# Kernel optimization log

Measured on AMD Instinct MI355X. Metric: run time of the kernel, lower is better.

## Reference

```python
import jax, jax.numpy as jnp
from jax import lax
import numpy as np

EPS = 1e-5
ALPHA = 0.2  # LeakyReLU slope


def setup_inputs() -> dict:
    key = jax.random.key(0)
    ks = jax.random.split(key, 8)
    B, N, F_IN, HID, OUT, H = 32, 512, 256, 512, 512, 4
    D = OUT // H
    return {
        "x": jax.random.normal(ks[0], (B, N, F_IN), dtype=jnp.float32),
        "adj": jax.random.uniform(ks[1], (N, N), dtype=jnp.float32),
        "gc_w": jax.random.normal(ks[2], (F_IN, HID), dtype=jnp.float32) * 0.04,
        "gc_b": jax.random.normal(ks[3], (HID,), dtype=jnp.float32) * 0.04,
        "bn1_g": jnp.ones((HID,), jnp.float32),
        "bn1_b": jnp.zeros((HID,), jnp.float32),
        "bn1_m": jnp.zeros((HID,), jnp.float32),
        "bn1_v": jnp.ones((HID,), jnp.float32),
        "gat_w": jax.random.normal(ks[4], (H, D, HID), dtype=jnp.float32) * 0.04,
        "conv_w": jax.random.normal(ks[5], (OUT, OUT, 3), dtype=jnp.float32) * 0.02,
        "conv_b": jax.random.normal(ks[6], (OUT,), dtype=jnp.float32) * 0.02,
        "bn2_g": jnp.ones((OUT,), jnp.float32),
        "bn2_b": jnp.zeros((OUT,), jnp.float32),
        "bn2_m": jnp.zeros((OUT,), jnp.float32),
        "bn2_v": jnp.ones((OUT,), jnp.float32),
    }


def reference(x, adj, gc_w, gc_b, bn1_g, bn1_b, bn1_m, bn1_v, gat_w,
              conv_w, conv_b, bn2_g, bn2_b, bn2_m, bn2_v):
    # --- GraphConvolution: adj @ (x @ W) + b ---
    support = jnp.einsum('bnc,cd->bnd', x, gc_w)
    g = jnp.einsum('nm,bmd->bnd', adj, support) + gc_b  # [B,N,HID]
    # --- BatchNorm1d over channel dim (eval mode) + ReLU ---
    g = (g - bn1_m) * (bn1_g / jnp.sqrt(bn1_v + EPS)) + bn1_b
    g = jax.nn.relu(g)
    # --- Multi-head GAT (repeat/mul/sum == attention-weighted matmul) ---
    hh = jnp.einsum('bnf,hdf->bhnd', g, gat_w)           # per-head projections
    e = jnp.einsum('bhnd,bhmd->bhnm', hh, hh)            # logits [B,H,N,N]
    e = jnp.where(e > 0, e, ALPHA * e)                   # LeakyReLU
    att = jax.nn.softmax(e, axis=-1)
    o = jnp.einsum('bhnm,bhmd->bhnd', att, hh)
    B, H, N, D = o.shape
    o = o.transpose(0, 2, 1, 3).reshape(B, N, H * D)     # concat heads [B,N,OUT]
    # --- TCN block: conv1d(k=3,pad=1) over node axis + BN(eval) + ReLU ---
    xc = o.transpose(0, 2, 1)                            # [B,C,N]
    y = lax.conv_general_dilated(xc, conv_w, (1,), ((1, 1),),
                                 dimension_numbers=('NCH', 'OIH', 'NCH'))
    y = y + conv_b[None, :, None]
    y = (y - bn2_m[None, :, None]) * (bn2_g / jnp.sqrt(bn2_v + EPS))[None, :, None] + bn2_b[None, :, None]
    y = jax.nn.relu(y)
    return y.transpose(0, 2, 1)                          # [B,N,OUT]
```

## Files before the change

kernel.cpp:

```cpp
#include <hip/hip_runtime.h>
#include <math.h>

#define BATCH 32
#define NNODE 512
#define FIN   256
#define HIDC  512
#define OUTC  512
#define NHEAD 4
#define HDIM  128
#define EPSV  1e-5f
#define ALPHA_LR 0.2f

typedef _Float16 half8 __attribute__((ext_vector_type(8)));
typedef _Float16 half4v __attribute__((ext_vector_type(4)));
typedef float floatx4 __attribute__((ext_vector_type(4)));

#define GLOBAL_TO_LDS16(g, l)                                                  \
  __builtin_amdgcn_global_load_lds(                                            \
      (const __attribute__((address_space(1))) void*)(g),                      \
      (__attribute__((address_space(3))) void*)(l), 16, 0, 0)

__device__ __forceinline__ void split_gemm_acc(
    const _Float16* __restrict__ Ah, const _Float16* __restrict__ Al, int lda,
    const _Float16* __restrict__ Bh, const _Float16* __restrict__ Bl, int ldb,
    int K, int rowBase, int colBase,
    _Float16* sAh, _Float16* sAl, _Float16* sBh, _Float16* sBl,
    floatx4 acc[4][4], int tid) {
  const int lane = tid & 63, wave = tid >> 6;
  const int wr = (wave >> 1) * 64, wc = (wave & 1) * 64;
  const int fr = lane & 15, q = lane >> 4;
  const int r = tid >> 2, ko = (tid & 3) * 8;
  for (int k0 = 0; k0 < K; k0 += 32) {
    GLOBAL_TO_LDS16(&Ah[(size_t)(rowBase + r) * lda + k0 + ko], &sAh[tid * 8]);
    GLOBAL_TO_LDS16(&Ah[(size_t)(rowBase + r + 64) * lda + k0 + ko], &sAh[2048 + tid * 8]);
    GLOBAL_TO_LDS16(&Al[(size_t)(rowBase + r) * lda + k0 + ko], &sAl[tid * 8]);
    GLOBAL_TO_LDS16(&Al[(size_t)(rowBase + r + 64) * lda + k0 + ko], &sAl[2048 + tid * 8]);
    GLOBAL_TO_LDS16(&Bh[(size_t)(colBase + r) * ldb + k0 + ko], &sBh[tid * 8]);
    GLOBAL_TO_LDS16(&Bh[(size_t)(colBase + r + 64) * ldb + k0 + ko], &sBh[2048 + tid * 8]);
    GLOBAL_TO_LDS16(&Bl[(size_t)(colBase + r) * ldb + k0 + ko], &sBl[tid * 8]);
    GLOBAL_TO_LDS16(&Bl[(size_t)(colBase + r + 64) * ldb + k0 + ko], &sBl[2048 + tid * 8]);
    __syncthreads();
    half8 ah[4], al4[4], bh[4], bl4[4];
#pragma unroll
    for (int i = 0; i < 4; ++i) {
      ah[i]  = *(const half8*)&sAh[(wr + i * 16 + fr) * 32 + q * 8];
      al4[i] = *(const half8*)&sAl[(wr + i * 16 + fr) * 32 + q * 8];
    }
#pragma unroll
    for (int j = 0; j < 4; ++j) {
      bh[j]  = *(const half8*)&sBh[(wc + j * 16 + fr) * 32 + q * 8];
      bl4[j] = *(const half8*)&sBl[(wc + j * 16 + fr) * 32 + q * 8];
    }
#pragma unroll
    for (int i = 0; i < 4; ++i)
#pragma unroll
      for (int j = 0; j < 4; ++j) {
        acc[i][j] = __builtin_amdgcn_mfma_f32_16x16x32_f16(al4[i], bh[j], acc[i][j], 0, 0, 0);
        acc[i][j] = __builtin_amdgcn_mfma_f32_16x16x32_f16(ah[i], bl4[j], acc[i][j], 0, 0, 0);
        acc[i][j] = __builtin_amdgcn_mfma_f32_16x16x32_f16(ah[i], bh[j], acc[i][j], 0, 0, 0);
      }
    __syncthreads();
  }
}

__global__ __launch_bounds__(256) void k_prep(
    const float* __restrict__ adj, const float* __restrict__ gcw,
    const float* __restrict__ gatw, const float* __restrict__ cw,
    _Float16* __restrict__ ADJh, _Float16* __restrict__ ADJl,
    _Float16* __restrict__ GWh, _Float16* __restrict__ GWl,
    _Float16* __restrict__ GAh, _Float16* __restrict__ GAl,
    _Float16* __restrict__ WT, _Float16* __restrict__ OP) {
  const int i = blockIdx.x * 256 + threadIdx.x;
  if (i < 262144) {
    float v = adj[i];
    _Float16 h = (_Float16)v;
    ADJh[i] = h; ADJl[i] = (_Float16)(v - (float)h);
  } else if (i < 393216) {
    int j = i - 262144;
    int n = j >> 8, k = j & 255;
    float v = gcw[(size_t)k * HIDC + n];
    _Float16 h = (_Float16)v;
    GWh[j] = h; GWl[j] = (_Float16)(v - (float)h);
  } else if (i < 655360) {
    int j = i - 393216;
    float v = gatw[j];
    _Float16 h = (_Float16)v;
    GAh[j] = h; GAl[j] = (_Float16)(v - (float)h);
  } else if (i < 1441792) {
    int j = i - 655360;
    int n = j / 1536, kk = j - n * 1536;
    int tap = kk >> 9, ci = kk & 511;
    WT[j] = (_Float16)cw[(size_t)n * 1536 + ci * 3 + tap];
  } else if (i < 1474560) {
    int j = i - 1441792;
    int b = j >> 10, rs = (j >> 9) & 1, c = j & 511;
    OP[((size_t)b * 514 + rs * 513) * OUTC + c] = (_Float16)0.f;
  }
}

__global__ __launch_bounds__(256) void k_xsplit(const float* __restrict__ X,
                                                _Float16* __restrict__ Xh,
                                                _Float16* __restrict__ Xl) {
  const int i = (blockIdx.x * 256 + threadIdx.x) * 4;
  float4 v = *(const float4*)&X[i];
  half4v h, l;
  h[0] = (_Float16)v.x; l[0] = (_Float16)(v.x - (float)h[0]);
  h[1] = (_Float16)v.y; l[1] = (_Float16)(v.y - (float)h[1]);
  h[2] = (_Float16)v.z; l[2] = (_Float16)(v.z - (float)h[2]);
  h[3] = (_Float16)v.w; l[3] = (_Float16)(v.w - (float)h[3]);
  *(half4v*)&Xh[i] = h;
  *(half4v*)&Xl[i] = l;
}

__global__ __launch_bounds__(256) void k_support_t(
    const _Float16* __restrict__ GWh, const _Float16* __restrict__ GWl,
    const _Float16* __restrict__ Xh, const _Float16* __restrict__ Xl,
    _Float16* __restrict__ STh, _Float16* __restrict__ STl) {
  __shared__ _Float16 sm[4][4096];
  const int tid = threadIdx.x;
  const int rowBase = blockIdx.y * 128, colBase = blockIdx.x * 128;
  floatx4 acc[4][4] = {};
  split_gemm_acc(GWh, GWl, FIN, Xh, Xl, FIN, FIN, rowBase, colBase,
                 sm[0], sm[1], sm[2], sm[3], acc, tid);
  const int lane = tid & 63, wave = tid >> 6;
  const int wr = (wave >> 1) * 64, wc = (wave & 1) * 64;
  const int fr = lane & 15, q = lane >> 4;
#pragma unroll
  for (int i = 0; i < 4; ++i) {
    const int ch0 = rowBase + wr + i * 16 + q * 4;
#pragma unroll
    for (int rg = 0; rg < 4; ++rg) {
      size_t base = (size_t)(ch0 + rg) * 16384 + colBase + wc + fr;
#pragma unroll
      for (int j = 0; j < 4; ++j) {
        float v = acc[i][j][rg];
        _Float16 h = (_Float16)v;
        STh[base + j * 16] = h;
        STl[base + j * 16] = (_Float16)(v - (float)h);
      }
    }
  }
}

__global__ __launch_bounds__(256) void k_gcn(
    const _Float16* __restrict__ ADJh, const _Float16* __restrict__ ADJl,
    const _Float16* __restrict__ STh, const _Float16* __restrict__ STl,
    const float* __restrict__ gcb, const float* __restrict__ g1,
    const float* __restrict__ b1, const float* __restrict__ m1,
    const float* __restrict__ v1,
    _Float16* __restrict__ Gh, _Float16* __restrict__ Gl) {
  __shared__ _Float16 sm[4][4096];
  const int tid = threadIdx.x;
  const int rowBase = blockIdx.y * 128, colBase = blockIdx.x * 128;
  const int b = blockIdx.z;
  floatx4 acc[4][4] = {};
  split_gemm_acc(ADJh, ADJl, NNODE, STh + (size_t)b * NNODE, STl + (size_t)b * NNODE,
                 16384, NNODE, rowBase, colBase, sm[0], sm[1], sm[2], sm[3], acc, tid);
  const int lane = tid & 63, wave = tid >> 6;
  const int wr = (wave >> 1) * 64, wc = (wave & 1) * 64;
  const int fr = lane & 15, q = lane >> 4;
  float sc[4], of[4];
#pragma unroll
  for (int j = 0; j < 4; ++j) {
    int c = colBase + wc + j * 16 + fr;
    float s = g1[c] * rsqrtf(v1[c] + EPSV);
    sc[j] = s;
    of[j] = (gcb[c] - m1[c]) * s + b1[c];
  }
#pragma unroll
  for (int i = 0; i < 4; ++i) {
    const int n0 = rowBase + wr + i * 16 + q * 4;
#pragma unroll
    for (int rg = 0; rg < 4; ++rg) {
      size_t base = ((size_t)b * NNODE + n0 + rg) * HIDC + colBase + wc + fr;
#pragma unroll
      for (int j = 0; j < 4; ++j) {
        float v = fmaxf(fmaf(acc[i][j][rg], sc[j], of[j]), 0.0f);
        _Float16 h = (_Float16)v;
        Gh[base + j * 16] = h;
        Gl[base + j * 16] = (_Float16)(v - (float)h);
      }
    }
  }
}

__global__ __launch_bounds__(256) void k_hh(
    const _Float16* __restrict__ Gh, const _Float16* __restrict__ Gl,
    const _Float16* __restrict__ GAh, const _Float16* __restrict__ GAl,
    _Float16* __restrict__ HHh, _Float16* __restrict__ HHl) {
  __shared__ _Float16 sm[4][4096];
  const int tid = threadIdx.x;
  const int rowBase = blockIdx.y * 128, colBase = blockIdx.x * 128;
  floatx4 acc[4][4] = {};
  split_gemm_acc(Gh, Gl, HIDC, GAh, GAl, HIDC, HIDC, rowBase, colBase,
                 sm[0], sm[1], sm[2], sm[3], acc, tid);
  const int lane = tid & 63, wave = tid >> 6;
  const int wr = (wave >> 1) * 64, wc = (wave & 1) * 64;
  const int fr = lane & 15, q = lane >> 4;
#pragma unroll
  for (int i = 0; i < 4; ++i) {
    const int r0 = rowBase + wr + i * 16 + q * 4;
#pragma unroll
    for (int rg = 0; rg < 4; ++rg) {
      size_t base = (size_t)(r0 + rg) * OUTC + colBase + wc + fr;
#pragma unroll
      for (int j = 0; j < 4; ++j) {
        float v = acc[i][j][rg];
        _Float16 h = (_Float16)v;
        HHh[base + j * 16] = h;
        HHl[base + j * 16] = (_Float16)(v - (float)h);
      }
    }
  }
}

__global__ __launch_bounds__(256) void k_vt(const _Float16* __restrict__ HHh,
                                            _Float16* __restrict__ HHT) {
  __shared__ _Float16 sT[128 * 132];
  const int bt = blockIdx.x;
  const int nt = bt & 3, g = bt >> 2;
  const int bb = g >> 2, h = g & 3;
  const int tid = threadIdx.x;
  const int rr = tid >> 4, cc = (tid & 15) * 8;
#pragma unroll
  for (int it = 0; it < 8; ++it) {
    int node = rr + it * 16;
    half8 v = *(const half8*)&HHh[((size_t)bb * 512 + nt * 128 + node) * 512 + h * 128 + cc];
#pragma unroll
    for (int e = 0; e < 8; ++e) sT[(cc + e) * 132 + node] = v[e];
  }
  __syncthreads();
#pragma unroll
  for (int it = 0; it < 8; ++it) {
    int d = rr + it * 16;
    half8 v;
#pragma unroll
    for (int e = 0; e < 8; ++e) v[e] = sT[d * 132 + cc + e];
    *(half8*)&HHT[((size_t)g * 128 + d) * 512 + nt * 128 + cc] = v;
  }
}

__global__ __launch_bounds__(256, 3) void k_attn(
    const _Float16* __restrict__ HHh, const _Float16* __restrict__ HHl,
    const _Float16* __restrict__ HHT, _Float16* __restrict__ OP) {
  __shared__ _Float16 sKh[128 * 32], sKl[128 * 32];
  __shared__ _Float16 sV[128 * 32];
  __shared__ _Float16 sP[64 * 44];
  const int tid = threadIdx.x;
  const int lane = tid & 63, wave = tid >> 6;
  const int fr = lane & 15, q = lane >> 4;
  const int id = blockIdx.x;
  const int slot = id >> 3;
  const int g = (id & 7) + 8 * (slot >> 3);
  const int qBase = (slot & 7) * 64;
  const int bb = g >> 2, h = g & 3;
  const int w16 = wave * 16;
  const _Float16* Qh = HHh + (size_t)bb * NNODE * OUTC + h * HDIM;
  const _Float16* Ql = HHl + (size_t)bb * NNODE * OUTC + h * HDIM;
  const _Float16* VT = HHT + (size_t)g * HDIM * NNODE;
  const int r = tid >> 2, ko = (tid & 3) * 8;

  half8 qh[4], ql[4];
#pragma unroll
  for (int k0 = 0; k0 < 4; ++k0) {
    const size_t off = (size_t)(qBase + w16 + fr) * OUTC + k0 * 32 + q * 8;
    qh[k0] = *(const half8*)&Qh[off];
    ql[k0] = *(const half8*)&Ql[off];
  }

  floatx4 oacc[8] = {};
  float m_i[4], l_i[4];
#pragma unroll
  for (int rg = 0; rg < 4; ++rg) { m_i[rg] = -1e30f; l_i[rg] = 0.f; }

  for (int kt = 0; kt < 4; ++kt) {
    const int ktb = kt * 128;
    floatx4 sacc[8] = {};
#pragma unroll
    for (int k0 = 0; k0 < 4; ++k0) {
      GLOBAL_TO_LDS16(&Qh[(size_t)(ktb + r) * OUTC + k0 * 32 + ko], &sKh[tid * 8]);
      GLOBAL_TO_LDS16(&Qh[(size_t)(ktb + r + 64) * OUTC + k0 * 32 + ko], &sKh[2048 + tid * 8]);
      GLOBAL_TO_LDS16(&Ql[(size_t)(ktb + r) * OUTC + k0 * 32 + ko], &sKl[tid * 8]);
      GLOBAL_TO_LDS16(&Ql[(size_t)(ktb + r + 64) * OUTC + k0 * 32 + ko], &sKl[2048 + tid * 8]);
      __syncthreads();
#pragma unroll
      for (int j = 0; j < 8; ++j) {
        half8 bh = *(const half8*)&sKh[(j * 16 + fr) * 32 + q * 8];
        half8 bl = *(const half8*)&sKl[(j * 16 + fr) * 32 + q * 8];
        sacc[j] = __builtin_amdgcn_mfma_f32_16x16x32_f16(ql[k0], bh, sacc[j], 0, 0, 0);
        sacc[j] = __builtin_amdgcn_mfma_f32_16x16x32_f16(qh[k0], bl, sacc[j], 0, 0, 0);
        sacc[j] = __builtin_amdgcn_mfma_f32_16x16x32_f16(qh[k0], bh, sacc[j], 0, 0, 0);
      }
      __syncthreads();
    }
#pragma unroll
    for (int j = 0; j < 8; ++j)
#pragma unroll
      for (int rg = 0; rg < 4; ++rg) {
        float v = sacc[j][rg];
        sacc[j][rg] = v > 0.f ? v : ALPHA_LR * v;
      }
#pragma unroll
    for (int rg = 0; rg < 4; ++rg) {
      float mx = sacc[0][rg];
#pragma unroll
      for (int j = 1; j < 8; ++j) mx = fmaxf(mx, sacc[j][rg]);
      mx = fmaxf(mx, __shfl_xor(mx, 1));
      mx = fmaxf(mx, __shfl_xor(mx, 2));
      mx = fmaxf(mx, __shfl_xor(mx, 4));
      mx = fmaxf(mx, __shfl_xor(mx, 8));
      float mnew = fmaxf(m_i[rg], mx);
      float alpha = __expf(m_i[rg] - mnew);
      m_i[rg] = mnew;
      float sum = 0.f;
#pragma unroll
      for (int j = 0; j < 8; ++j) {
        float p = __expf(sacc[j][rg] - mnew);
        sacc[j][rg] = p;
        sum += p;
      }
      sum += __shfl_xor(sum, 1);
      sum += __shfl_xor(sum, 2);
      sum += __shfl_xor(sum, 4);
      sum += __shfl_xor(sum, 8);
      l_i[rg] = l_i[rg] * alpha + sum;
#pragma unroll
      for (int j = 0; j < 8; ++j) oacc[j][rg] *= alpha;
    }
#pragma unroll
    for (int ks = 0; ks < 4; ++ks) {
#pragma unroll
      for (int jj = 0; jj < 2; ++jj)
#pragma unroll
        for (int rg = 0; rg < 4; ++rg)
          sP[(w16 + q * 4 + rg) * 44 + jj * 16 + fr] = (_Float16)sacc[2 * ks + jj][rg];
      GLOBAL_TO_LDS16(&VT[(size_t)r * NNODE + ktb + ks * 32 + ko], &sV[tid * 8]);
      GLOBAL_TO_LDS16(&VT[(size_t)(r + 64) * NNODE + ktb + ks * 32 + ko], &sV[2048 + tid * 8]);
      __syncthreads();
      half8 pa = *(const half8*)&sP[(w16 + fr) * 44 + q * 8];
#pragma unroll
      for (int j = 0; j < 8; ++j) {
        half8 bv = *(const half8*)&sV[(j * 16 + fr) * 32 + q * 8];
        oacc[j] = __builtin_amdgcn_mfma_f32_16x16x32_f16(pa, bv, oacc[j], 0, 0, 0);
      }
      __syncthreads();
    }
  }
#pragma unroll
  for (int rg = 0; rg < 4; ++rg) {
    const float inv = 1.0f / l_i[rg];
    const int node = qBase + w16 + q * 4 + rg;
    size_t base = ((size_t)bb * 514 + 1 + node) * OUTC + h * HDIM + fr;
#pragma unroll
    for (int j = 0; j < 8; ++j)
      OP[base + j * 16] = (_Float16)(oacc[j][rg] * inv);
  }
}

__global__ __launch_bounds__(256) void k_conv_mfma(
    const _Float16* __restrict__ OP, const _Float16* __restrict__ WT,
    const float* __restrict__ cb, const float* __restrict__ g2,
    const float* __restrict__ b2, const float* __restrict__ m2,
    const float* __restrict__ v2, float* __restrict__ Y) {
  __shared__ _Float16 At[128 * 32];
  __shared__ _Float16 Bt[128 * 32];
  const int tid = threadIdx.x;
  const int lane = tid & 63, wave = tid >> 6;
  const int wr = (wave >> 1) * 64, wc = (wave & 1) * 64;
  const int id = blockIdx.y * 4 + blockIdx.x;
  const int jj = id >> 3;
  const int rowBase = ((id & 7) * 16 + (jj >> 2)) * 128;
  const int colBase = (jj & 3) * 128;
  const int b = rowBase >> 9;
  const int n0 = rowBase & 511;
  const int r = tid >> 2;
  const int ko = (tid & 3) * 8;
  floatx4 acc[4][4] = {};
  for (int k0 = 0; k0 < 3 * OUTC; k0 += 32) {
    const int tap = k0 >> 9;
    const int cib = k0 & 511;
    const size_t abase = ((size_t)b * 514 + n0 + tap) * OUTC + cib + ko;
    GLOBAL_TO_LDS16(&OP[abase + (size_t)r * OUTC],        &At[tid * 8]);
    GLOBAL_TO_LDS16(&OP[abase + (size_t)(r + 64) * OUTC], &At[2048 + tid * 8]);
    GLOBAL_TO_LDS16(&WT[(size_t)(colBase + r) * 1536 + k0 + ko],      &Bt[tid * 8]);
    GLOBAL_TO_LDS16(&WT[(size_t)(colBase + r + 64) * 1536 + k0 + ko], &Bt[2048 + tid * 8]);
    __syncthreads();
    const int fr = lane & 15, q = lane >> 4;
    half8 af[4], bf[4];
#pragma unroll
    for (int i = 0; i < 4; ++i)
      af[i] = *(const half8*)&At[(wr + i * 16 + fr) * 32 + q * 8];
#pragma unroll
    for (int j = 0; j < 4; ++j)
      bf[j] = *(const half8*)&Bt[(wc + j * 16 + fr) * 32 + q * 8];
#pragma unroll
    for (int i = 0; i < 4; ++i)
#pragma unroll
      for (int j = 0; j < 4; ++j)
        acc[i][j] = __builtin_amdgcn_mfma_f32_16x16x32_f16(af[i], bf[j], acc[i][j], 0, 0, 0);
    __syncthreads();
  }
  const int fr = lane & 15, q = lane >> 4;
  float sc[4], of[4];
#pragma unroll
  for (int j = 0; j < 4; ++j) {
    int c = colBase + wc + j * 16 + fr;
    float s = g2[c] * rsqrtf(v2[c] + EPSV);
    sc[j] = s;
    of[j] = (cb[c] - m2[c]) * s + b2[c];
  }
#pragma unroll
  for (int i = 0; i < 4; ++i) {
    const int R0r = rowBase + wr + i * 16 + q * 4;
#pragma unroll
    for (int rg = 0; rg < 4; ++rg) {
      float* dst = &Y[(size_t)(R0r + rg) * OUTC + colBase + wc + fr];
#pragma unroll
      for (int j = 0; j < 4; ++j)
        dst[j * 16] = fmaxf(fmaf(acc[i][j][rg], sc[j], of[j]), 0.0f);
    }
  }
}

extern "C" void kernel_launch(void* const* d_in, const int* in_sizes, int n_in,
                              void* d_out, int out_size, void* d_ws, size_t ws_size,
                              hipStream_t stream) {
  const float* x     = (const float*)d_in[0];
  const float* adj   = (const float*)d_in[1];
  const float* gc_w  = (const float*)d_in[2];
  const float* gc_b  = (const float*)d_in[3];
  const float* bn1_g = (const float*)d_in[4];
  const float* bn1_b = (const float*)d_in[5];
  const float* bn1_m = (const float*)d_in[6];
  const float* bn1_v = (const float*)d_in[7];
  const float* gat_w = (const float*)d_in[8];
  const float* conv_w= (const float*)d_in[9];
  const float* conv_b= (const float*)d_in[10];
  const float* bn2_g = (const float*)d_in[11];
  const float* bn2_b = (const float*)d_in[12];
  const float* bn2_m = (const float*)d_in[13];
  const float* bn2_v = (const float*)d_in[14];
  float* out = (float*)d_out;

  char* ws = (char*)d_ws;
  _Float16* STh = (_Float16*)(ws + 0);
  _Float16* STl = (_Float16*)(ws + 16777216);
  _Float16* HHh = (_Float16*)(ws + 0);
  _Float16* HHl = (_Float16*)(ws + 16777216);
  _Float16* Xh  = (_Float16*)(ws + 33554432);
  _Float16* Xl  = (_Float16*)(ws + 41943040);
  _Float16* Gh  = (_Float16*)(ws + 33554432);
  _Float16* Gl  = (_Float16*)(ws + 50331648);
  _Float16* HHT = (_Float16*)(ws + 33554432);
  _Float16* OP  = (_Float16*)(ws + 67108864);
  _Float16* WT  = (_Float16*)(ws + 83951616);
  _Float16* ADJh= (_Float16*)(ws + 85524480);
  _Float16* ADJl= (_Float16*)(ws + 86048768);
  _Float16* GWh = (_Float16*)(ws + 86573056);
  _Float16* GWl = (_Float16*)(ws + 86835200);
  _Float16* GAh = (_Float16*)(ws + 87097344);
  _Float16* GAl = (_Float16*)(ws + 87621632);

  k_prep<<<5760, 256, 0, stream>>>(adj, gc_w, gat_w, conv_w,
                                   ADJh, ADJl, GWh, GWl, GAh, GAl, WT, OP);
  k_xsplit<<<4096, 256, 0, stream>>>(x, Xh, Xl);
  k_support_t<<<dim3(128, 4), 256, 0, stream>>>(GWh, GWl, Xh, Xl, STh, STl);
  k_gcn<<<dim3(4, 4, 32), 256, 0, stream>>>(ADJh, ADJl, STh, STl, gc_b,
                                            bn1_g, bn1_b, bn1_m, bn1_v, Gh, Gl);
  k_hh<<<dim3(4, 128), 256, 0, stream>>>(Gh, Gl, GAh, GAl, HHh, HHl);
  k_vt<<<512, 256, 0, stream>>>(HHh, HHT);
  k_attn<<<1024, 256, 0, stream>>>(HHh, HHl, HHT, OP);
  k_conv_mfma<<<dim3(4, 128), 256, 0, stream>>>(OP, WT, conv_b,
                                                bn2_g, bn2_b, bn2_m, bn2_v, out);
}
```

Before: 299.8 us.

## Restructure attention kernel to 64-key tiles with fewer barriers per tile

The flash-attention kernel now processes 64 keys per outer iteration instead of 128. It loads the entire K hi/lo slice for all four depth chunks in one shot and reuses that LDS region for V. This cuts the number of __syncthreads per key tile from about 16 to 4 and shrinks the score accumulator registers. The trade-off is twice as many online-softmax rescale steps and a different LDS footprint (32KB for K plus a wider P buffer), which may affect occupancy at 3 blocks per CU.

```diff
diff --git a/kernel.cpp b/kernel.cpp
--- a/kernel.cpp
+++ b/kernel.cpp
@@ -243,9 +243,9 @@
 __global__ __launch_bounds__(256, 3) void k_attn(
     const _Float16* __restrict__ HHh, const _Float16* __restrict__ HHl,
     const _Float16* __restrict__ HHT, _Float16* __restrict__ OP) {
-  __shared__ _Float16 sKh[128 * 32], sKl[128 * 32];
-  __shared__ _Float16 sV[128 * 32];
-  __shared__ _Float16 sP[64 * 44];
+  __shared__ _Float16 sK[8][2048];
+  __shared__ _Float16 sP[64 * 68];
+  _Float16* sV = &sK[0][0];
   const int tid = threadIdx.x;
   const int lane = tid & 63, wave = tid >> 6;
   const int fr = lane & 15, q = lane >> 4;
@@ -258,7 +258,7 @@
   const _Float16* Qh = HHh + (size_t)bb * NNODE * OUTC + h * HDIM;
   const _Float16* Ql = HHl + (size_t)bb * NNODE * OUTC + h * HDIM;
   const _Float16* VT = HHT + (size_t)g * HDIM * NNODE;
-  const int r = tid >> 2, ko = (tid & 3) * 8;
+  const int rk = tid >> 2, ck = (tid & 3) * 8;
 
   half8 qh[4], ql[4];
 #pragma unroll
@@ -273,28 +273,28 @@
 #pragma unroll
   for (int rg = 0; rg < 4; ++rg) { m_i[rg] = -1e30f; l_i[rg] = 0.f; }
 
-  for (int kt = 0; kt < 4; ++kt) {
-    const int ktb = kt * 128;
-    floatx4 sacc[8] = {};
-#pragma unroll
-    for (int k0 = 0; k0 < 4; ++k0) {
-      GLOBAL_TO_LDS16(&Qh[(size_t)(ktb + r) * OUTC + k0 * 32 + ko], &sKh[tid * 8]);
-      GLOBAL_TO_LDS16(&Qh[(size_t)(ktb + r + 64) * OUTC + k0 * 32 + ko], &sKh[2048 + tid * 8]);
-      GLOBAL_TO_LDS16(&Ql[(size_t)(ktb + r) * OUTC + k0 * 32 + ko], &sKl[tid * 8]);
-      GLOBAL_TO_LDS16(&Ql[(size_t)(ktb + r + 64) * OUTC + k0 * 32 + ko], &sKl[2048 + tid * 8]);
-      __syncthreads();
-#pragma unroll
-      for (int j = 0; j < 8; ++j) {
-        half8 bh = *(const half8*)&sKh[(j * 16 + fr) * 32 + q * 8];
-        half8 bl = *(const half8*)&sKl[(j * 16 + fr) * 32 + q * 8];
+  for (int kt = 0; kt < 8; ++kt) {
+    const int ktb = kt * 64;
+#pragma unroll
+    for (int t = 0; t < 4; ++t) {
+      GLOBAL_TO_LDS16(&Qh[(size_t)(ktb + rk) * OUTC + t * 32 + ck], &sK[t][tid * 8]);
+      GLOBAL_TO_LDS16(&Ql[(size_t)(ktb + rk) * OUTC + t * 32 + ck], &sK[4 + t][tid * 8]);
+    }
+    __syncthreads();
+    floatx4 sacc[4] = {};
+#pragma unroll
+    for (int k0 = 0; k0 < 4; ++k0)
+#pragma unroll
+      for (int j = 0; j < 4; ++j) {
+        half8 bh = *(const half8*)&sK[k0][(j * 16 + fr) * 32 + q * 8];
+        half8 bl = *(const half8*)&sK[4 + k0][(j * 16 + fr) * 32 + q * 8];
         sacc[j] = __builtin_amdgcn_mfma_f32_16x16x32_f16(ql[k0], bh, sacc[j], 0, 0, 0);
         sacc[j] = __builtin_amdgcn_mfma_f32_16x16x32_f16(qh[k0], bl, sacc[j], 0, 0, 0);
         sacc[j] = __builtin_amdgcn_mfma_f32_16x16x32_f16(qh[k0], bh, sacc[j], 0, 0, 0);
       }
-      __syncthreads();
-    }
-#pragma unroll
-    for (int j = 0; j < 8; ++j)
+    __syncthreads();
+#pragma unroll
+    for (int j = 0; j < 4; ++j)
 #pragma unroll
       for (int rg = 0; rg < 4; ++rg) {
         float v = sacc[j][rg];
@@ -304,7 +304,7 @@
     for (int rg = 0; rg < 4; ++rg) {
       float mx = sacc[0][rg];
 #pragma unroll
-      for (int j = 1; j < 8; ++j) mx = fmaxf(mx, sacc[j][rg]);
+      for (int j = 1; j < 4; ++j) mx = fmaxf(mx, sacc[j][rg]);
       mx = fmaxf(mx, __shfl_xor(mx, 1));
       mx = fmaxf(mx, __shfl_xor(mx, 2));
       mx = fmaxf(mx, __shfl_xor(mx, 4));
@@ -314,7 +314,7 @@
       m_i[rg] = mnew;
       float sum = 0.f;
 #pragma unroll
-      for (int j = 0; j < 8; ++j) {
+      for (int j = 0; j < 4; ++j) {
         float p = __expf(sacc[j][rg] - mnew);
         sacc[j][rg] = p;
         sum += p;
@@ -328,23 +328,25 @@
       for (int j = 0; j < 8; ++j) oacc[j][rg] *= alpha;
     }
 #pragma unroll
-    for (int ks = 0; ks < 4; ++ks) {
-#pragma unroll
-      for (int jj = 0; jj < 2; ++jj)
-#pragma unroll
-        for (int rg = 0; rg < 4; ++rg)
-          sP[(w16 + q * 4 + rg) * 44 + jj * 16 + fr] = (_Float16)sacc[2 * ks + jj][rg];
-      GLOBAL_TO_LDS16(&VT[(size_t)r * NNODE + ktb + ks * 32 + ko], &sV[tid * 8]);
-      GLOBAL_TO_LDS16(&VT[(size_t)(r + 64) * NNODE + ktb + ks * 32 + ko], &sV[2048 + tid * 8]);
-      __syncthreads();
-      half8 pa = *(const half8*)&sP[(w16 + fr) * 44 + q * 8];
+    for (int l = 0; l < 4; ++l)
+      GLOBAL_TO_LDS16(&VT[(size_t)((l >> 1) * 64 + rk) * NNODE + ktb + (l & 1) * 32 + ck],
+                      &sV[(l & 1) * 4096 + (l >> 1) * 2048 + tid * 8]);
+#pragma unroll
+    for (int j = 0; j < 4; ++j)
+#pragma unroll
+      for (int rg = 0; rg < 4; ++rg)
+        sP[(w16 + q * 4 + rg) * 68 + j * 16 + fr] = (_Float16)sacc[j][rg];
+    __syncthreads();
+#pragma unroll
+    for (int ks = 0; ks < 2; ++ks) {
+      half8 pa = *(const half8*)&sP[(w16 + fr) * 68 + ks * 32 + q * 8];
 #pragma unroll
       for (int j = 0; j < 8; ++j) {
-        half8 bv = *(const half8*)&sV[(j * 16 + fr) * 32 + q * 8];
+        half8 bv = *(const half8*)&sV[ks * 4096 + (j * 16 + fr) * 32 + q * 8];
         oacc[j] = __builtin_amdgcn_mfma_f32_16x16x32_f16(pa, bv, oacc[j], 0, 0, 0);
       }
-      __syncthreads();
-    }
+    }
+    __syncthreads();
   }
 #pragma unroll
   for (int rg = 0; rg < 4; ++rg) {
```

New measurement: 293.5 us. -2.1%, faster.
